# Optimization experiments

Measured on AMD Instinct MI355X. Metric: run time of the kernel, lower is better.

Reference implementation:

```python
import jax, jax.numpy as jnp
import numpy as np

B, S, D, F, E, K = 2, 2048, 1024, 1024, 8, 2


def setup_inputs() -> dict:
    key = jax.random.key(0)
    kx, kg, k1, k3, k2 = jax.random.split(key, 5)
    # kaiming_uniform_(a=sqrt(5)) => Uniform(-1/sqrt(fan_in), 1/sqrt(fan_in))
    x = jax.random.normal(kx, (B, S, D), dtype=jnp.float32)
    gate_w = jax.random.uniform(kg, (E, D), jnp.float32, -1.0, 1.0) / np.sqrt(D)
    w1 = jax.random.uniform(k1, (E, F, D), jnp.float32, -1.0, 1.0) / np.sqrt(D)
    w3 = jax.random.uniform(k3, (E, F, D), jnp.float32, -1.0, 1.0) / np.sqrt(D)
    w2 = jax.random.uniform(k2, (E, D, F), jnp.float32, -1.0, 1.0) / np.sqrt(F)
    return {"x": x, "gate_w": gate_w, "w1": w1, "w3": w3, "w2": w2}


def reference(x, gate_w, w1, w3, w2):
    b, s, d = x.shape
    T = b * s
    xf = x.reshape(T, d)                      # [T, D]
    # ---- Gate: softmax scores, top-k selection, renormalized weights ----
    logits = xf @ gate_w.T                    # [T, E]
    probs = jax.nn.softmax(logits, axis=-1)
    topk_w, topk_idx = jax.lax.top_k(probs, K)            # [T, K]
    topk_w = topk_w / jnp.sum(topk_w, axis=-1, keepdims=True)
    # Dense per-token gate matrix [T, E]; zero for unselected experts, so the
    # weighted combine below is exactly sum_k w_k * expert_{idx_k}(x).
    gate_full = jnp.zeros((T, E), x.dtype).at[
        jnp.arange(T)[:, None], topk_idx].add(topk_w)
    # ---- Grouped SwiGLU experts: loop over small fixed E, vectorized over tokens ----
    out = jnp.zeros_like(xf)
    for e in range(E):
        h = jax.nn.silu(xf @ w1[e].T) * (xf @ w3[e].T)    # [T, F]
        out = out + gate_full[:, e:e + 1] * (h @ w2[e].T)  # [T, D]
    return out.reshape(b, s, d)
```

## Files before the change

kernel.cpp:

```cpp
#include <hip/hip_runtime.h>
#include <hip/hip_bf16.h>
#include <cstdint>
#include <cstddef>

#define T_TOK 4096
#define DDIM  1024
#define FDIM  1024
#define NEXP  8

typedef __attribute__((ext_vector_type(8))) short bf16x8;
typedef __attribute__((ext_vector_type(4))) float f32x4;
typedef __attribute__((ext_vector_type(8))) unsigned short u16x8;

__device__ __forceinline__ unsigned short f2bf(float f) {
  unsigned int u = __float_as_uint(f);
  u += 0x7FFFu + ((u >> 16) & 1u);
  return (unsigned short)(u >> 16);
}
__device__ __forceinline__ float bf2f(unsigned short u) {
  return __uint_as_float(((unsigned int)u) << 16);
}

__device__ __forceinline__ void gload_lds16(const void* g, void* l) {
  __builtin_amdgcn_global_load_lds(
      (const __attribute__((address_space(1))) unsigned int*)g,
      (__attribute__((address_space(3))) unsigned int*)l, 16, 0, 0);
}

__device__ __forceinline__ void vwait6() { asm volatile("s_waitcnt vmcnt(6)" ::: "memory"); }
__device__ __forceinline__ void vwait4() { asm volatile("s_waitcnt vmcnt(4)" ::: "memory"); }
__device__ __forceinline__ void vwait0() { asm volatile("s_waitcnt vmcnt(0)" ::: "memory"); }
__device__ __forceinline__ void lwait0() { asm volatile("s_waitcnt lgkmcnt(0)" ::: "memory"); }
__device__ __forceinline__ void barr()   { asm volatile("s_barrier" ::: "memory"); }

__device__ __forceinline__ bf16x8 frag_ld(const unsigned short* tile, int row, int kk) {
  int byteoff = (row << 7) + ((kk * 2) ^ ((row & 7) << 4));
  return *reinterpret_cast<const bf16x8*>(reinterpret_cast<const char*>(tile) + byteoff);
}

__global__ __launch_bounds__(256) void prep_kernel(
    const float* __restrict__ w1, const float* __restrict__ w3,
    unsigned short* __restrict__ W1b, unsigned short* __restrict__ W3b,
    const float* __restrict__ x, const float* __restrict__ gw,
    unsigned int* __restrict__ Xb32, int* __restrict__ tkidx, float* __restrict__ tkw,
    int* __restrict__ curp) {
  __shared__ float gws[NEXP * DDIM];
  const int bid = blockIdx.x;
  const int tid = threadIdx.x;

  if (bid < 2048) {
    const int sub = bid >> 10;
    const int b = bid & 1023;
    const float* s = (sub == 0) ? w1 : w3;
    unsigned short* d = (sub == 0) ? W1b : W3b;
    const int n = NEXP * FDIM * DDIM;
    const int stride = 1024 * 256 * 8;
    for (int i = (b * 256 + tid) * 8; i < n; i += stride) {
      float4 a = *reinterpret_cast<const float4*>(s + i);
      float4 c = *reinterpret_cast<const float4*>(s + i + 4);
      u16x8 o;
      o[0] = f2bf(a.x); o[1] = f2bf(a.y); o[2] = f2bf(a.z); o[3] = f2bf(a.w);
      o[4] = f2bf(c.x); o[5] = f2bf(c.y); o[6] = f2bf(c.z); o[7] = f2bf(c.w);
      *reinterpret_cast<u16x8*>(d + i) = o;
    }
    return;
  }

  const int lane = tid & 63;
  const int wid = tid >> 6;
  if (bid == 2048 && tid < NEXP) curp[tid * 32] = 0;
  for (int i = tid; i < NEXP * DDIM / 4; i += 256)
    reinterpret_cast<float4*>(gws)[i] = reinterpret_cast<const float4*>(gw)[i];
  __syncthreads();

  const int t = (bid - 2048) * 4 + wid;
  const float2* xr = reinterpret_cast<const float2*>(x + (size_t)t * DDIM);
  float2 xv[8];
#pragma unroll
  for (int i = 0; i < 8; ++i) xv[i] = xr[i * 64 + lane];
#pragma unroll
  for (int i = 0; i < 8; ++i)
    Xb32[(size_t)t * 512 + i * 64 + lane] =
        (unsigned int)f2bf(xv[i].x) | ((unsigned int)f2bf(xv[i].y) << 16);
  float p[NEXP];
#pragma unroll
  for (int e = 0; e < NEXP; ++e) p[e] = 0.f;
#pragma unroll
  for (int i = 0; i < 8; ++i) {
    const int k = (i * 64 + lane) * 2;
#pragma unroll
    for (int e = 0; e < NEXP; ++e)
      p[e] += xv[i].x * gws[e * DDIM + k] + xv[i].y * gws[e * DDIM + k + 1];
  }
#pragma unroll
  for (int s = 32; s > 0; s >>= 1)
#pragma unroll
    for (int e = 0; e < NEXP; ++e) p[e] += __shfl_xor(p[e], s, 64);
  if (lane == 0) {
    int i0 = 0; float l0 = p[0];
#pragma unroll
    for (int e = 1; e < NEXP; ++e) if (p[e] > l0) { l0 = p[e]; i0 = e; }
    int i1 = -1; float l1 = -1e30f;
#pragma unroll
    for (int e = 0; e < NEXP; ++e) if (e != i0 && p[e] > l1) { l1 = p[e]; i1 = e; }
    float ex = __expf(l1 - l0);
    float w0 = 1.f / (1.f + ex);
    float w1v = ex / (1.f + ex);
    tkidx[t * 2] = i0; tkidx[t * 2 + 1] = i1;
    tkw[t * 2] = w0;   tkw[t * 2 + 1] = w1v;
  }
}

__global__ __launch_bounds__(256) void fill_kernel(const int* __restrict__ tkidx,
                                                   const float* __restrict__ tkw,
                                                   int* __restrict__ offp,
                                                   int* __restrict__ curp,
                                                   int* __restrict__ list,
                                                   float* __restrict__ rgate,
                                                   int* __restrict__ wmap,
                                                   int* __restrict__ nwp) {
  __shared__ int ghist[4][NEXP];
  __shared__ int lhist[NEXP], base[NEXP];
  const int tid = threadIdx.x;
  if (tid < 32) ghist[tid >> 3][tid & 7] = 0;
  if (tid < NEXP) lhist[tid] = 0;
  __syncthreads();
  for (int i = tid; i < 2 * T_TOK; i += 256)
    atomicAdd(&ghist[tid >> 6][tkidx[i]], 1);
  const int t = blockIdx.x * 256 + tid;
  const int e0 = tkidx[t * 2], e1 = tkidx[t * 2 + 1];
  const int r0 = atomicAdd(&lhist[e0], 1);
  const int r1 = atomicAdd(&lhist[e1], 1);
  __syncthreads();
  if (blockIdx.x == 0 && tid == 64) {
    int nw = 0;
    for (int e = 0; e < NEXP; ++e) {
      int c = ghist[0][e] + ghist[1][e] + ghist[2][e] + ghist[3][e];
      int nrt = (c + 127) >> 7;
      for (int r = 0; r < nrt; ++r) wmap[nw++] = (e << 8) | r;
    }
    nwp[0] = nw;
  }
  if (tid < NEXP) {
    int o = 0;
#pragma unroll
    for (int j = 0; j < NEXP; ++j) {
      int c = ghist[0][j] + ghist[1][j] + ghist[2][j] + ghist[3][j];
      if (j < tid) o += c;
    }
    if (blockIdx.x == 0) {
      offp[tid] = o;
      if (tid == NEXP - 1)
        offp[NEXP] = o + ghist[0][tid] + ghist[1][tid] + ghist[2][tid] + ghist[3][tid];
    }
    base[tid] = o + atomicAdd(&curp[tid * 32], lhist[tid]);
  }
  __syncthreads();
  const int p0 = base[e0] + r0;
  const int p1 = base[e1] + r1;
  list[p0] = (t << 1);     rgate[p0] = tkw[t * 2];
  list[p1] = (t << 1) | 1; rgate[p1] = tkw[t * 2 + 1];
}

__global__ __launch_bounds__(256) void gemm1_kernel(
    const unsigned short* __restrict__ Xb, const unsigned short* __restrict__ W1b,
    const unsigned short* __restrict__ W3b, unsigned short* __restrict__ Hb,
    const int* __restrict__ off, const int* __restrict__ list,
    const int* __restrict__ wmap, const int* __restrict__ nwp,
    const float* __restrict__ w2, unsigned short* __restrict__ W2b) {
  const int bid0 = blockIdx.x;
  const int tid = threadIdx.x;

  if (bid0 >= 72 * 16) {
    const int b = bid0 - 72 * 16;
    const int n = NEXP * FDIM * DDIM;
    const int stride = 1024 * 256 * 8;
    for (int i = (b * 256 + tid) * 8; i < n; i += stride) {
      float4 a = *reinterpret_cast<const float4*>(w2 + i);
      float4 c = *reinterpret_cast<const float4*>(w2 + i + 4);
      u16x8 o;
      o[0] = f2bf(a.x); o[1] = f2bf(a.y); o[2] = f2bf(a.z); o[3] = f2bf(a.w);
      o[4] = f2bf(c.x); o[5] = f2bf(c.y); o[6] = f2bf(c.z); o[7] = f2bf(c.w);
      *reinterpret_cast<u16x8*>(W2b + i) = o;
    }
    return;
  }

  const int slot = bid0 >> 4;
  const int ft = bid0 & 15;
  if (slot >= nwp[0]) return;
  const int ent = wmap[slot];
  const int e = ent >> 8;
  const int rt = ent & 255;
  const int seg0 = off[e];
  const int Ne = off[e + 1] - seg0;
  const int rowbase = rt * 128;
  const int f0 = ft * 64;

  __shared__ unsigned short As[2][128 * 64];
  __shared__ unsigned short B1s[64 * 64];
  __shared__ unsigned short B3s[64 * 64];

  const int lane = tid & 63;
  const int wid = tid >> 6;
  const int wr = wid >> 1, wc = wid & 1;

  int ldsoffA[4]; size_t abase[4];
#pragma unroll
  for (int j = 0; j < 4; ++j) {
    int boff = j * 4096 + wid * 1024 + lane * 16;
    int row = boff >> 7;
    int c = ((boff >> 4) & 7) ^ (row & 7);
    ldsoffA[j] = (j * 4096 + wid * 1024) >> 1;
    int ar = rowbase + row; if (ar > Ne - 1) ar = Ne - 1;
    int tok = list[seg0 + ar] >> 1;
    abase[j] = (size_t)tok * DDIM + c * 8;
  }
  size_t bsrc[2]; int ldsWB[2];
#pragma unroll
  for (int j = 0; j < 2; ++j) {
    int boff = j * 4096 + wid * 1024 + lane * 16;
    int row = boff >> 7;
    int c = ((boff >> 4) & 7) ^ (row & 7);
    ldsWB[j] = boff >> 1;
    bsrc[j] = (size_t)(e * FDIM + f0 + row) * DDIM + c * 8;
  }

  f32x4 acc1[4][2], acc3[4][2];
  const f32x4 z = {0.f, 0.f, 0.f, 0.f};
#pragma unroll
  for (int m = 0; m < 4; ++m)
#pragma unroll
    for (int n = 0; n < 2; ++n) { acc1[m][n] = z; acc3[m][n] = z; }

  const int lrow = lane & 15;
  const int kb = (lane >> 4) * 8;

  vwait0();
#pragma unroll
  for (int j = 0; j < 4; ++j)
    gload_lds16(Xb + abase[j], &As[0][ldsoffA[j]]);
  bf16x8 bc1[2], bc3[2], bn1[2], bn3[2];
#pragma unroll
  for (int j = 0; j < 2; ++j) {
    bc1[j] = *reinterpret_cast<const bf16x8*>(W1b + bsrc[j]);
    bc3[j] = *reinterpret_cast<const bf16x8*>(W3b + bsrc[j]);
  }
  vwait4();

#pragma unroll 2
  for (int kt = 0; kt < 16; ++kt) {
    const int cur = kt & 1;
    if (kt < 15) {
      const int ko = (kt + 1) * 64;
#pragma unroll
      for (int j = 0; j < 4; ++j)
        gload_lds16(Xb + abase[j] + ko, &As[cur ^ 1][ldsoffA[j]]);
#pragma unroll
      for (int j = 0; j < 2; ++j) {
        bn1[j] = *reinterpret_cast<const bf16x8*>(W1b + bsrc[j] + ko);
        bn3[j] = *reinterpret_cast<const bf16x8*>(W3b + bsrc[j] + ko);
      }
    }
#pragma unroll
    for (int j = 0; j < 2; ++j) {
      *reinterpret_cast<bf16x8*>(&B1s[ldsWB[j]]) = bc1[j];
      *reinterpret_cast<bf16x8*>(&B3s[ldsWB[j]]) = bc3[j];
    }
    lwait0();
    barr();
#pragma unroll
    for (int ks = 0; ks < 2; ++ks) {
      bf16x8 a[4], p[2], q[2];
#pragma unroll
      for (int m = 0; m < 4; ++m)
        a[m] = frag_ld(As[cur], wr * 64 + m * 16 + lrow, ks * 32 + kb);
#pragma unroll
      for (int n = 0; n < 2; ++n) {
        p[n] = frag_ld(B1s, wc * 32 + n * 16 + lrow, ks * 32 + kb);
        q[n] = frag_ld(B3s, wc * 32 + n * 16 + lrow, ks * 32 + kb);
      }
#pragma unroll
      for (int m = 0; m < 4; ++m)
#pragma unroll
        for (int n = 0; n < 2; ++n) {
          acc1[m][n] = __builtin_amdgcn_mfma_f32_16x16x32_bf16(a[m], p[n], acc1[m][n], 0, 0, 0);
          acc3[m][n] = __builtin_amdgcn_mfma_f32_16x16x32_bf16(a[m], q[n], acc3[m][n], 0, 0, 0);
        }
    }
    if (kt == 15) break;
    vwait4();
    barr();
#pragma unroll
    for (int j = 0; j < 2; ++j) { bc1[j] = bn1[j]; bc3[j] = bn3[j]; }
  }

#pragma unroll
  for (int m = 0; m < 4; ++m)
#pragma unroll
    for (int n = 0; n < 2; ++n)
#pragma unroll
      for (int r = 0; r < 4; ++r) {
        int rloc = wr * 64 + m * 16 + ((lane >> 4) << 2) + r;
        if (rowbase + rloc < Ne) {
          float v1 = acc1[m][n][r], v3 = acc3[m][n][r];
          float h = v1 / (1.f + __expf(-v1)) * v3;
          int col = f0 + wc * 32 + n * 16 + (lane & 15);
          Hb[(size_t)(seg0 + rowbase + rloc) * FDIM + col] = f2bf(h);
        }
      }
}

__global__ __launch_bounds__(256) void gemm2_kernel(
    const unsigned short* __restrict__ Hb, const unsigned short* __restrict__ W2b,
    unsigned short* __restrict__ Yb, const int* __restrict__ off,
    const int* __restrict__ list, const float* __restrict__ rgate,
    const int* __restrict__ wmap, const int* __restrict__ nwp) {
  const int bid0 = blockIdx.x;
  const int slot = bid0 >> 4;
  const int dt = bid0 & 15;
  if (slot >= nwp[0]) return;
  const int ent = wmap[slot];
  const int e = ent >> 8;
  const int rt = ent & 255;
  const int seg0 = off[e];
  const int Ne = off[e + 1] - seg0;
  const int rowbase = rt * 128;
  const int d0 = dt * 64;

  __shared__ unsigned short As[2][128 * 64];
  __shared__ unsigned short Bs[2][64 * 64];

  const int tid = threadIdx.x;
  const int lane = tid & 63;
  const int wid = tid >> 6;
  const int wr = wid >> 1, wc = wid & 1;

  int ldsoffA[4]; size_t abase[4];
  int ldsoffB[2]; size_t bbase[2];
#pragma unroll
  for (int j = 0; j < 4; ++j) {
    int boff = j * 4096 + wid * 1024 + lane * 16;
    int row = boff >> 7;
    int c = ((boff >> 4) & 7) ^ (row & 7);
    ldsoffA[j] = (j * 4096 + wid * 1024) >> 1;
    int ar = rowbase + row; if (ar > Ne - 1) ar = Ne - 1;
    abase[j] = (size_t)(seg0 + ar) * FDIM + c * 8;
  }
#pragma unroll
  for (int j = 0; j < 2; ++j) {
    int boff = j * 4096 + wid * 1024 + lane * 16;
    int row = boff >> 7;
    int c = ((boff >> 4) & 7) ^ (row & 7);
    ldsoffB[j] = (j * 4096 + wid * 1024) >> 1;
    bbase[j] = (size_t)(e * DDIM + d0 + row) * FDIM + c * 8;
  }

  f32x4 acc[4][2];
  const f32x4 z = {0.f, 0.f, 0.f, 0.f};
#pragma unroll
  for (int m = 0; m < 4; ++m)
#pragma unroll
    for (int n = 0; n < 2; ++n) acc[m][n] = z;

  auto stage = [&](int buf, int kt) {
    const int ko = kt * 64;
#pragma unroll
    for (int j = 0; j < 4; ++j)
      gload_lds16(Hb + abase[j] + ko, &As[buf][ldsoffA[j]]);
#pragma unroll
    for (int j = 0; j < 2; ++j)
      gload_lds16(W2b + bbase[j] + ko, &Bs[buf][ldsoffB[j]]);
  };

  const int lrow = lane & 15;
  const int kb = (lane >> 4) * 8;

  vwait0();
  stage(0, 0);
  stage(1, 1);
  vwait6();
  barr();

  for (int t = 0; t < 16; ++t) {
    const int b = t & 1;
#pragma unroll
    for (int ks = 0; ks < 2; ++ks) {
      bf16x8 a[4], bb[2];
#pragma unroll
      for (int m = 0; m < 4; ++m)
        a[m] = frag_ld(As[b], wr * 64 + m * 16 + lrow, ks * 32 + kb);
#pragma unroll
      for (int n = 0; n < 2; ++n)
        bb[n] = frag_ld(Bs[b], wc * 32 + n * 16 + lrow, ks * 32 + kb);
#pragma unroll
      for (int m = 0; m < 4; ++m)
#pragma unroll
        for (int n = 0; n < 2; ++n)
          acc[m][n] = __builtin_amdgcn_mfma_f32_16x16x32_bf16(a[m], bb[n], acc[m][n], 0, 0, 0);
    }
    if (t == 15) break;
    lwait0();
    barr();
    if (t + 2 < 16) stage(b, t + 2);
    if (t < 14) vwait6(); else vwait0();
    barr();
  }

#pragma unroll
  for (int m = 0; m < 4; ++m)
#pragma unroll
    for (int r = 0; r < 4; ++r) {
      int rloc = wr * 64 + m * 16 + ((lane >> 4) << 2) + r;
      if (rowbase + rloc < Ne) {
        int rg = seg0 + rowbase + rloc;
        int tk = list[rg];
        float gsc = rgate[rg];
#pragma unroll
        for (int n = 0; n < 2; ++n) {
          int col = d0 + wc * 32 + n * 16 + (lane & 15);
          Yb[(size_t)tk * DDIM + col] = f2bf(gsc * acc[m][n][r]);
        }
      }
    }
}

__global__ __launch_bounds__(256) void combine_kernel(const unsigned short* __restrict__ Yb,
                                                      float* __restrict__ out) {
  const int n = T_TOK * DDIM / 8;
  const int stride = gridDim.x * blockDim.x;
  for (int i = blockIdx.x * blockDim.x + threadIdx.x; i < n; i += stride) {
    int t = i >> 7;
    int c = (i & 127) * 8;
    u16x8 a = *reinterpret_cast<const u16x8*>(Yb + ((size_t)t * 2) * DDIM + c);
    u16x8 b = *reinterpret_cast<const u16x8*>(Yb + ((size_t)t * 2 + 1) * DDIM + c);
    float4 o0, o1;
    o0.x = bf2f(a[0]) + bf2f(b[0]); o0.y = bf2f(a[1]) + bf2f(b[1]);
    o0.z = bf2f(a[2]) + bf2f(b[2]); o0.w = bf2f(a[3]) + bf2f(b[3]);
    o1.x = bf2f(a[4]) + bf2f(b[4]); o1.y = bf2f(a[5]) + bf2f(b[5]);
    o1.z = bf2f(a[6]) + bf2f(b[6]); o1.w = bf2f(a[7]) + bf2f(b[7]);
    float* dst = out + (size_t)t * DDIM + c;
    *reinterpret_cast<float4*>(dst) = o0;
    *reinterpret_cast<float4*>(dst + 4) = o1;
  }
}

extern "C" void kernel_launch(void* const* d_in, const int* in_sizes, int n_in,
                              void* d_out, int out_size, void* d_ws, size_t ws_size,
                              hipStream_t stream) {
  (void)in_sizes; (void)n_in; (void)ws_size; (void)out_size;
  const float* x  = (const float*)d_in[0];
  const float* gw = (const float*)d_in[1];
  const float* w1 = (const float*)d_in[2];
  const float* w3 = (const float*)d_in[3];
  const float* w2 = (const float*)d_in[4];
  float* out = (float*)d_out;

  char* ws = (char*)d_ws;
  unsigned short* Xb  = (unsigned short*)(ws + 0);
  unsigned short* W1b = (unsigned short*)(ws + 8388608);
  unsigned short* W3b = (unsigned short*)(ws + 25165824);
  unsigned short* W2b = (unsigned short*)(ws + 41943040);
  unsigned short* Hb  = (unsigned short*)(ws + 58720256);
  unsigned short* Yb  = (unsigned short*)(ws + 8388608);
  int*   ctrl  = (int*)(ws + 75497472);
  int*   off   = ctrl;
  int*   nwp   = ctrl + 12;
  int*   curp  = ctrl + 16;
  int*   wmap  = ctrl + 256;
  int*   tkidx = (int*)(ws + 75497472 + 4096);
  float* tkw   = (float*)(ws + 75497472 + 4096 + 32768);
  int*   list  = (int*)(ws + 75497472 + 4096 + 65536);
  float* rgate = (float*)(ws + 75497472 + 4096 + 98304);

  prep_kernel<<<3072, 256, 0, stream>>>(w1, w3, W1b, W3b,
                                        x, gw, (unsigned int*)Xb, tkidx, tkw, curp);
  fill_kernel<<<16, 256, 0, stream>>>(tkidx, tkw, off, curp, list, rgate, wmap, nwp);

  gemm1_kernel<<<72 * 16 + 1024, 256, 0, stream>>>(Xb, W1b, W3b, Hb, off, list,
                                                   wmap, nwp, w2, W2b);
  gemm2_kernel<<<72 * 16, 256, 0, stream>>>(Hb, W2b, Yb, off, list, rgate, wmap, nwp);
  combine_kernel<<<2048, 256, 0, stream>>>(Yb, out);
}
```

Baseline: 161.0 us.

## Replace double-buffered gate/up GEMM loop with single-buffer direct-to-LDS loads

The gate/up projection kernel drops its double-buffered A tile and register-staged B prefetch. Each k-step now issues global_load_lds for X, W1 and W3 straight into single LDS buffers, then synchronises, computes and synchronises again. This removes the register staging and the LDS store instructions for B, but loads no longer overlap with MFMA compute inside a block. It also relies on __syncthreads to cover the outstanding direct-to-LDS loads.

```diff
diff --git a/kernel.cpp b/kernel.cpp
--- a/kernel.cpp
+++ b/kernel.cpp
@@ -28,7 +28,6 @@
 }
 
 __device__ __forceinline__ void vwait6() { asm volatile("s_waitcnt vmcnt(6)" ::: "memory"); }
-__device__ __forceinline__ void vwait4() { asm volatile("s_waitcnt vmcnt(4)" ::: "memory"); }
 __device__ __forceinline__ void vwait0() { asm volatile("s_waitcnt vmcnt(0)" ::: "memory"); }
 __device__ __forceinline__ void lwait0() { asm volatile("s_waitcnt lgkmcnt(0)" ::: "memory"); }
 __device__ __forceinline__ void barr()   { asm volatile("s_barrier" ::: "memory"); }
@@ -197,7 +196,7 @@
   const int rowbase = rt * 128;
   const int f0 = ft * 64;
 
-  __shared__ unsigned short As[2][128 * 64];
+  __shared__ unsigned short As[128 * 64];
   __shared__ unsigned short B1s[64 * 64];
   __shared__ unsigned short B3s[64 * 64];
 
@@ -206,6 +205,7 @@
   const int wr = wid >> 1, wc = wid & 1;
 
   int ldsoffA[4]; size_t abase[4];
+  int ldsoffB[2]; size_t b1base[2];
 #pragma unroll
   for (int j = 0; j < 4; ++j) {
     int boff = j * 4096 + wid * 1024 + lane * 16;
@@ -216,14 +216,13 @@
     int tok = list[seg0 + ar] >> 1;
     abase[j] = (size_t)tok * DDIM + c * 8;
   }
-  size_t bsrc[2]; int ldsWB[2];
 #pragma unroll
   for (int j = 0; j < 2; ++j) {
     int boff = j * 4096 + wid * 1024 + lane * 16;
     int row = boff >> 7;
     int c = ((boff >> 4) & 7) ^ (row & 7);
-    ldsWB[j] = boff >> 1;
-    bsrc[j] = (size_t)(e * FDIM + f0 + row) * DDIM + c * 8;
+    ldsoffB[j] = (j * 4096 + wid * 1024) >> 1;
+    b1base[j] = (size_t)(e * FDIM + f0 + row) * DDIM + c * 8;
   }
 
   f32x4 acc1[4][2], acc3[4][2];
@@ -235,46 +234,23 @@
 
   const int lrow = lane & 15;
   const int kb = (lane >> 4) * 8;
-
-  vwait0();
-#pragma unroll
-  for (int j = 0; j < 4; ++j)
-    gload_lds16(Xb + abase[j], &As[0][ldsoffA[j]]);
-  bf16x8 bc1[2], bc3[2], bn1[2], bn3[2];
-#pragma unroll
-  for (int j = 0; j < 2; ++j) {
-    bc1[j] = *reinterpret_cast<const bf16x8*>(W1b + bsrc[j]);
-    bc3[j] = *reinterpret_cast<const bf16x8*>(W3b + bsrc[j]);
-  }
-  vwait4();
-
-#pragma unroll 2
-  for (int kt = 0; kt < 16; ++kt) {
-    const int cur = kt & 1;
-    if (kt < 15) {
-      const int ko = (kt + 1) * 64;
-#pragma unroll
-      for (int j = 0; j < 4; ++j)
-        gload_lds16(Xb + abase[j] + ko, &As[cur ^ 1][ldsoffA[j]]);
-#pragma unroll
-      for (int j = 0; j < 2; ++j) {
-        bn1[j] = *reinterpret_cast<const bf16x8*>(W1b + bsrc[j] + ko);
-        bn3[j] = *reinterpret_cast<const bf16x8*>(W3b + bsrc[j] + ko);
-      }
-    }
+  for (int kt = 0; kt < DDIM / 64; ++kt) {
+    const int ko = kt * 64;
+#pragma unroll
+    for (int j = 0; j < 4; ++j)
+      gload_lds16(Xb + abase[j] + ko, &As[ldsoffA[j]]);
 #pragma unroll
     for (int j = 0; j < 2; ++j) {
-      *reinterpret_cast<bf16x8*>(&B1s[ldsWB[j]]) = bc1[j];
-      *reinterpret_cast<bf16x8*>(&B3s[ldsWB[j]]) = bc3[j];
-    }
-    lwait0();
-    barr();
+      gload_lds16(W1b + b1base[j] + ko, &B1s[ldsoffB[j]]);
+      gload_lds16(W3b + b1base[j] + ko, &B3s[ldsoffB[j]]);
+    }
+    __syncthreads();
 #pragma unroll
     for (int ks = 0; ks < 2; ++ks) {
       bf16x8 a[4], p[2], q[2];
 #pragma unroll
       for (int m = 0; m < 4; ++m)
-        a[m] = frag_ld(As[cur], wr * 64 + m * 16 + lrow, ks * 32 + kb);
+        a[m] = frag_ld(As, wr * 64 + m * 16 + lrow, ks * 32 + kb);
 #pragma unroll
       for (int n = 0; n < 2; ++n) {
         p[n] = frag_ld(B1s, wc * 32 + n * 16 + lrow, ks * 32 + kb);
@@ -288,11 +264,7 @@
           acc3[m][n] = __builtin_amdgcn_mfma_f32_16x16x32_bf16(a[m], q[n], acc3[m][n], 0, 0, 0);
         }
     }
-    if (kt == 15) break;
-    vwait4();
-    barr();
-#pragma unroll
-    for (int j = 0; j < 2; ++j) { bc1[j] = bn1[j]; bc3[j] = bn3[j]; }
+    __syncthreads();
   }
 
 #pragma unroll
```

After: 133.3 us. 17.2% less time.
